# Performance work log

Hardware: AMD Instinct MI355X
Metric: run time of the kernel (lower is better)

## Reference

```python
import jax, jax.numpy as jnp
import numpy as np
from math import factorial

LMAX = 4
L2 = (LMAX + 1) ** 2                      # 25 spherical components
RES_B = 2 * (2 * LMAX + 1)                # 18 Gauss-Legendre beta nodes (exact for band 2*lmax products)
RES_A = 2 * (2 * LMAX + 1) + 1            # 19 uniform alpha nodes
EPS = 1e-5
# degree index of each (l,m) slot: [0,1,1,1,2,...]
L_IDX = np.repeat(np.arange(LMAX + 1), 2 * np.arange(LMAX + 1) + 1)


def _assoc_legendre(lmax, x):
    # Associated Legendre P_l^m(x) with Condon-Shortley phase; returns [l, m, B]
    B = x.shape[0]
    P = np.zeros((lmax + 1, lmax + 1, B))
    P[0, 0] = 1.0
    sx = np.sqrt(np.maximum(0.0, 1.0 - x * x))
    for m in range(1, lmax + 1):
        P[m, m] = -(2 * m - 1) * sx * P[m - 1, m - 1]
    for m in range(lmax):
        P[m + 1, m] = (2 * m + 1) * x * P[m, m]
    for m in range(lmax + 1):
        for l in range(m + 2, lmax + 1):
            P[l, m] = ((2 * l - 1) * x * P[l - 1, m] - (l + m - 1) * P[l - 2, m]) / (l - m)
    return P


def _build_sh(lmax, res_b, res_a):
    # Real orthonormal spherical harmonics sampled on a Gauss-Legendre x uniform-phi grid.
    ct, wb = np.polynomial.legendre.leggauss(res_b)       # cos(theta) nodes / weights
    phi = np.arange(res_a) * (2.0 * np.pi / res_a)
    P = _assoc_legendre(lmax, ct)
    l2 = (lmax + 1) ** 2
    Y = np.zeros((res_b, res_a, l2))
    for l in range(lmax + 1):
        for m in range(l + 1):
            Nlm = np.sqrt((2 * l + 1) / (4.0 * np.pi) * factorial(l - m) / factorial(l + m))
            if m == 0:
                Y[:, :, l * l + l] = (Nlm * P[l, 0])[:, None]
            else:
                base = np.sqrt(2.0) * Nlm * P[l, m]
                Y[:, :, l * l + l + m] = base[:, None] * np.cos(m * phi)[None, :]
                Y[:, :, l * l + l - m] = base[:, None] * np.sin(m * phi)[None, :]
    w = (wb[:, None] * np.full((1, res_a), 2.0 * np.pi / res_a)).reshape(-1)
    Yf = Y.reshape(-1, l2)
    return Yf, w

_Y_np, _w_np = _build_sh(LMAX, RES_B, RES_A)
TO_GRID = jnp.asarray(_Y_np, dtype=jnp.float32)                     # [G, L2]
FROM_GRID = jnp.asarray((_w_np[:, None] * _Y_np).T, dtype=jnp.float32)  # [L2, G], exact SH projection


def setup_inputs() -> dict:
    key = jax.random.key(0)
    ks = jax.random.split(key, 8)
    N, C = 6000, 128
    x = jax.random.normal(ks[0], (N, L2, C), dtype=jnp.float32)
    batch = jax.random.randint(ks[1], (N,), 0, 77)
    s = 1.0 / np.sqrt(C)
    return {
        "x": x,
        "batch": batch,
        "norm_w": jnp.ones((LMAX + 1, C), dtype=jnp.float32),
        "norm_b": jnp.zeros((C,), dtype=jnp.float32),
        "w1": jax.random.normal(ks[2], (LMAX + 1, C, C), dtype=jnp.float32) * s,
        "b1": jax.random.normal(ks[3], (C,), dtype=jnp.float32) * 0.02,
        "w_tp": jax.random.normal(ks[4], (LMAX + 1, C), dtype=jnp.float32),
        "w2": jax.random.normal(ks[5], (LMAX + 1, C, C), dtype=jnp.float32) * s,
        "b2": jax.random.normal(ks[6], (C,), dtype=jnp.float32) * 0.02,
    }


def _merge_layer_norm(x, w, b):
    # x: [N, L2, C]; center l=0 over channels, RMS over all components+channels, per-(l,C) affine.
    mean0 = jnp.mean(x[:, 0:1, :], axis=-1, keepdims=True)
    xc = jnp.concatenate([x[:, 0:1, :] - mean0, x[:, 1:, :]], axis=1)
    var = jnp.mean(xc * xc, axis=(1, 2), keepdims=True)
    xn = xc * jax.lax.rsqrt(var + EPS)
    out = xn * w[L_IDX][None]                      # [N, L2, C]
    return jnp.concatenate([out[:, 0:1, :] + b, out[:, 1:, :]], axis=1)


def _so3_linear(x, w, b):
    # per-degree linear: w [lmax+1, out, in]; bias on l=0 only
    W = w[L_IDX]                                    # [L2, out, in]
    y = jnp.einsum('nlc,lkc->nlk', x, W)
    return jnp.concatenate([y[:, 0:1, :] + b, y[:, 1:, :]], axis=1)


def _gaunt_self_tp(x, w_tp):
    # Gaunt self tensor-product (depthwise): pointwise square on the sphere,
    # exact projection back to SH (Gaunt-coefficient contraction), per-(l,C) weight.
    g = jnp.einsum('nlc,gl->ngc', x, TO_GRID)       # [N, G, C] to-grid
    y = jnp.einsum('ngc,lg->nlc', g * g, FROM_GRID)  # [N, L2, C] from-grid
    return y * w_tp[L_IDX][None]


def reference(x, batch, norm_w, norm_b, w1, b1, w_tp, w2, b2):
    x_res = x
    h = _merge_layer_norm(x, norm_w, norm_b)
    h = _so3_linear(h, w1, b1)
    h = _gaunt_self_tp(h, w_tp)
    h = _so3_linear(h, w2, b2)
    return h + x_res  # ffn_shortcut is Identity (num_in == num_out)
```

## Files before the change

### kernel.cpp

```cpp
#include <hip/hip_runtime.h>
#include <math.h>

#define L2C 25
#define CH  128
#define NB  8
#define GLB 7
#define GLA 13
#define NG  91
#define GPAD 96
#define KPAD 32
#define HROWS 242

typedef short bf16x8 __attribute__((ext_vector_type(8)));
typedef int   i32x4  __attribute__((ext_vector_type(4)));
typedef float f32x4  __attribute__((ext_vector_type(4)));
typedef unsigned uint2v __attribute__((ext_vector_type(2)));

union frag_u { i32x4 i; bf16x8 h; };

__device__ inline short f2bf(float f) {
  union { float f; unsigned u; } v; v.f = f;
  unsigned r = (v.u + 0x7FFFu + ((v.u >> 16) & 1u)) >> 16;
  return (short)r;
}
__device__ inline unsigned cvt_pk_bf16(float lo, float hi) {
  unsigned r; asm("v_cvt_pk_bf16_f32 %0, %1, %2" : "=v"(r) : "v"(lo), "v"(hi)); return r;
}

__global__ void build_tables_kernel(short* __restrict__ toT, short* __restrict__ frT) {
  const int g = threadIdx.x;
  if (g >= GPAD) return;
  const double PI = 3.14159265358979323846;
  double Y[L2C];
  double wg = 0.0;
  if (g < NG) {
    const int b = g / GLA;
    const int a = g % GLA;
    double xx = cos(PI * (b + 0.75) / (GLB + 0.5));
    double pp = 1.0;
    for (int it = 0; it < 64; ++it) {
      double p0 = 1.0, p1 = xx;
      for (int j = 2; j <= GLB; ++j) { double p2 = ((2.0*j-1.0)*xx*p1 - (j-1.0)*p0)/j; p0 = p1; p1 = p2; }
      pp = GLB * (xx*p1 - p0) / (xx*xx - 1.0);
      xx -= p1 / pp;
    }
    { double p0 = 1.0, p1 = xx;
      for (int j = 2; j <= GLB; ++j) { double p2 = ((2.0*j-1.0)*xx*p1 - (j-1.0)*p0)/j; p0 = p1; p1 = p2; }
      pp = GLB * (xx*p1 - p0) / (xx*xx - 1.0); }
    const double wb = 2.0 / ((1.0 - xx*xx) * pp * pp);
    const double ct = xx;
    const double sx = sqrt(fmax(0.0, 1.0 - ct*ct));
    double P[5][5];
    P[0][0] = 1.0;
    for (int m = 1; m <= 4; ++m) P[m][m] = -(2.0*m - 1.0) * sx * P[m-1][m-1];
    for (int m = 0; m <= 3; ++m) P[m+1][m] = (2.0*m + 1.0) * ct * P[m][m];
    for (int m = 0; m <= 4; ++m)
      for (int l = m + 2; l <= 4; ++l)
        P[l][m] = ((2.0*l-1.0)*ct*P[l-1][m] - (l+m-1.0)*P[l-2][m]) / (l - m);
    const double fact[9] = {1,1,2,6,24,120,720,5040,40320};
    const double phi = (2.0*PI/GLA) * a;
    for (int l = 0; l <= 4; ++l)
      for (int m = 0; m <= l; ++m) {
        double Nlm = sqrt((2.0*l+1.0)/(4.0*PI) * fact[l-m]/fact[l+m]);
        if (m == 0) Y[l*l + l] = Nlm * P[l][0];
        else {
          double base = sqrt(2.0) * Nlm * P[l][m];
          Y[l*l + l + m] = base * cos((double)m * phi);
          Y[l*l + l - m] = base * sin((double)m * phi);
        }
      }
    wg = wb * (2.0*PI/GLA);
  }
  for (int l = 0; l < KPAD; ++l) {
    float tv = (g < NG && l < L2C) ? (float)Y[l] : 0.f;
    toT[g*KPAD + l] = f2bf(tv);
  }
  {
    const int hi = g >> 4, r = g & 15;
    const int ksv = hi >> 1, pa = hi & 1;
    const int lqv = r >> 2,  pb = r & 3;
    const int kg = ksv*32 + lqv*8 + pa*4 + pb;
    for (int l = 0; l < KPAD; ++l)
      frT[l*GPAD + kg] = (g < NG && l < L2C) ? f2bf((float)(wg * Y[l])) : (short)0;
  }
}

__global__ void convert_w_kernel(const float* __restrict__ w1, const float* __restrict__ w2,
                                 short* __restrict__ wb1, short* __restrict__ wb2) {
  const int i = blockIdx.x * 256 + threadIdx.x;
  if (i < 5*CH*CH) { wb1[i] = f2bf(w1[i]); wb2[i] = f2bf(w2[i]); }
}

__global__ __launch_bounds__(512, 4) void eqv3_fused8u(
    const float* __restrict__ x,
    const float* __restrict__ norm_w, const float* __restrict__ norm_b,
    const short* __restrict__ wb1, const float* __restrict__ b1,
    const float* __restrict__ w_tp,
    const short* __restrict__ wb2, const float* __restrict__ b2,
    const short* __restrict__ toT, const short* __restrict__ frT,
    float* __restrict__ out)
{
  __shared__ __align__(16) short u[32768];
  short (*hsh)[HROWS][8] = (short (*)[HROWS][8])u;
  short (*hg)[4][CH][8]  = (short (*)[4][CH][8])u;

  const int tid  = threadIdx.x;
  const int w    = tid >> 6;
  const int lane = tid & 63;
  const int l16  = lane & 15;
  const int lq   = lane >> 4;
  const long n0  = (long)blockIdx.x * NB;
  const int k    = w*16 + l16;

  constexpr int LDEG[L2C] = {0,1,1,1,2,2,2,2,2,3,3,3,3,3,3,3,4,4,4,4,4,4,4,4,4};
  constexpr int BROW[5]   = {0,16,48,96,160};
  constexpr int NT[5]     = {1,2,3,4,5};

  {
    const float4* x4 = (const float4*)(x + (n0 + w)*(long)(L2C*CH));
    float4 xv[13];
    float s0 = 0.f, s0q = 0.f, sq = 0.f;
    #pragma unroll
    for (int it = 0; it < 13; ++it) {
      const int j = it*64 + lane;
      if (j < 800) {
        xv[it] = x4[j];
        const float t = xv[it].x*xv[it].x + xv[it].y*xv[it].y + xv[it].z*xv[it].z + xv[it].w*xv[it].w;
        if (j < 32) { s0 += xv[it].x + xv[it].y + xv[it].z + xv[it].w; s0q += t; }
        else        sq += t;
      }
    }
    #pragma unroll
    for (int o = 1; o < 64; o <<= 1) {
      s0  += __shfl_xor(s0,  o, 64);
      s0q += __shfl_xor(s0q, o, 64);
      sq  += __shfl_xor(sq,  o, 64);
    }
    const float mean0 = s0 * (1.f/CH);
    const float var   = (sq + s0q - CH*mean0*mean0) * (1.f/(L2C*CH));
    const float rstd  = rsqrtf(var + 1e-5f);
    #pragma unroll
    for (int it = 0; it < 13; ++it) {
      const int j = it*64 + lane;
      if (j < 800) {
        const int s = j >> 5;
        const int d = (int)sqrtf((float)s + 0.5f);
        const int row = 8*(s + d) + w;
        const int c32 = j & 31;
        const int c0  = c32 * 4;
        const float4 nw4 = ((const float4*)norm_w)[d*32 + c32];
        float a0 = xv[it].x, a1 = xv[it].y, a2 = xv[it].z, a3 = xv[it].w;
        if (s == 0) {
          const float4 nb4 = ((const float4*)norm_b)[c32];
          a0 = (a0 - mean0)*rstd*nw4.x + nb4.x;
          a1 = (a1 - mean0)*rstd*nw4.y + nb4.y;
          a2 = (a2 - mean0)*rstd*nw4.z + nb4.z;
          a3 = (a3 - mean0)*rstd*nw4.w + nb4.w;
        } else {
          a0 *= rstd*nw4.x; a1 *= rstd*nw4.y; a2 *= rstd*nw4.z; a3 *= rstd*nw4.w;
        }
        uint2v pk; pk[0] = cvt_pk_bf16(a0, a1); pk[1] = cvt_pk_bf16(a2, a3);
        *(uint2v*)&hsh[c0 >> 3][row][c0 & 7] = pk;
      }
    }
  }
  __syncthreads();

  unsigned pk1[15][2];
  {
    const float b1k = b1[k];
    int t = 0;
    #pragma unroll
    for (int d = 0; d < 5; ++d) {
      frag_u B[4];
      #pragma unroll
      for (int ks = 0; ks < 4; ++ks)
        B[ks].i = *(const i32x4*)(wb1 + ((d*CH + k)*CH + ks*32 + lq*8));
      #pragma unroll
      for (int mt = 0; mt < NT[d]; ++mt, ++t) {
        f32x4 acc = {0.f, 0.f, 0.f, 0.f};
        #pragma unroll
        for (int ks = 0; ks < 4; ++ks) {
          const bf16x8 a = *(const bf16x8*)&hsh[ks*4 + lq][BROW[d] + mt*16 + l16][0];
          acc = __builtin_amdgcn_mfma_f32_16x16x32_bf16(a, B[ks].h, acc, 0, 0, 0);
        }
        const int sl = 2*mt + (lq >> 1);
        const float bb = ((d == 0) & (sl == 0)) ? b1k : 0.f;
        pk1[t][0] = cvt_pk_bf16(acc[0] + bb, acc[1] + bb);
        pk1[t][1] = cvt_pk_bf16(acc[2] + bb, acc[3] + bb);
      }
    }
  }
  __syncthreads();

  {
    const i32x4 z = {0,0,0,0};
    #pragma unroll
    for (int n = 0; n < NB; ++n) *(i32x4*)&hg[n][3][k][0] = z;
    int t = 0;
    #pragma unroll
    for (int d = 0; d < 5; ++d)
      #pragma unroll
      for (int mt = 0; mt < NT[d]; ++mt, ++t) {
        const int sl = 2*mt + (lq >> 1);
        if (sl <= 2*d) {
          const int s  = d*d + sl;
          const int nb = (lq & 1)*4;
          hg[nb+0][s >> 3][k][s & 7] = (short)(pk1[t][0] & 0xFFFFu);
          hg[nb+1][s >> 3][k][s & 7] = (short)(pk1[t][0] >> 16);
          hg[nb+2][s >> 3][k][s & 7] = (short)(pk1[t][1] & 0xFFFFu);
          hg[nb+3][s >> 3][k][s & 7] = (short)(pk1[t][1] >> 16);
        }
      }
  }

  frag_u Bh[NB];
  #pragma unroll
  for (int n = 0; n < NB; ++n)
    Bh[n].i = *(const i32x4*)&hg[n][lq][k][0];
  __syncthreads();

  {
    frag_u Ato[6];
    #pragma unroll
    for (int gt = 0; gt < 6; ++gt)
      Ato[gt].i = *(const i32x4*)(toT + (gt*16 + l16)*KPAD + lq*8);
    frag_u Afr[2][3];
    #pragma unroll
    for (int mt = 0; mt < 2; ++mt)
      #pragma unroll
      for (int ks = 0; ks < 3; ++ks)
        Afr[mt][ks].i = *(const i32x4*)(frT + (mt*16 + l16)*GPAD + ks*32 + lq*8);

    float wtp[2][4]; int hrowb[2][4];
    #pragma unroll
    for (int mt = 0; mt < 2; ++mt)
      #pragma unroll
      for (int i = 0; i < 4; ++i) {
        const int l = mt*16 + lq*4 + i;
        if (l < L2C) {
          const int d = LDEG[l];
          wtp[mt][i]   = w_tp[d*CH + k];
          hrowb[mt][i] = BROW[d] + (l - d*d)*NB;
        } else { wtp[mt][i] = 0.f; hrowb[mt][i] = -1; }
      }

    #pragma unroll
    for (int np = 0; np < 4; ++np) {
      const int nA = np, nB2 = np + 4;
      unsigned pA[6][2], pB[6][2];
      #pragma unroll
      for (int gt = 0; gt < 6; ++gt) {
        f32x4 aA = {0.f,0.f,0.f,0.f}, aB = {0.f,0.f,0.f,0.f};
        aA = __builtin_amdgcn_mfma_f32_16x16x32_bf16(Ato[gt].h, Bh[nA].h,  aA, 0, 0, 0);
        aB = __builtin_amdgcn_mfma_f32_16x16x32_bf16(Ato[gt].h, Bh[nB2].h, aB, 0, 0, 0);
        pA[gt][0] = cvt_pk_bf16(aA[0]*aA[0], aA[1]*aA[1]);
        pA[gt][1] = cvt_pk_bf16(aA[2]*aA[2], aA[3]*aA[3]);
        pB[gt][0] = cvt_pk_bf16(aB[0]*aB[0], aB[1]*aB[1]);
        pB[gt][1] = cvt_pk_bf16(aB[2]*aB[2], aB[3]*aB[3]);
      }
      f32x4 acc2A[2] = {{0.f,0.f,0.f,0.f},{0.f,0.f,0.f,0.f}};
      f32x4 acc2B[2] = {{0.f,0.f,0.f,0.f},{0.f,0.f,0.f,0.f}};
      #pragma unroll
      for (int ks = 0; ks < 3; ++ks) {
        frag_u BgA, BgB;
        BgA.i[0] = (int)pA[2*ks][0];   BgA.i[1] = (int)pA[2*ks][1];
        BgA.i[2] = (int)pA[2*ks+1][0]; BgA.i[3] = (int)pA[2*ks+1][1];
        BgB.i[0] = (int)pB[2*ks][0];   BgB.i[1] = (int)pB[2*ks][1];
        BgB.i[2] = (int)pB[2*ks+1][0]; BgB.i[3] = (int)pB[2*ks+1][1];
        acc2A[0] = __builtin_amdgcn_mfma_f32_16x16x32_bf16(Afr[0][ks].h, BgA.h, acc2A[0], 0, 0, 0);
        acc2A[1] = __builtin_amdgcn_mfma_f32_16x16x32_bf16(Afr[1][ks].h, BgA.h, acc2A[1], 0, 0, 0);
        acc2B[0] = __builtin_amdgcn_mfma_f32_16x16x32_bf16(Afr[0][ks].h, BgB.h, acc2B[0], 0, 0, 0);
        acc2B[1] = __builtin_amdgcn_mfma_f32_16x16x32_bf16(Afr[1][ks].h, BgB.h, acc2B[1], 0, 0, 0);
      }
      #pragma unroll
      for (int mt = 0; mt < 2; ++mt)
        #pragma unroll
        for (int i = 0; i < 4; ++i)
          if (hrowb[mt][i] >= 0) {
            hsh[k >> 3][hrowb[mt][i] + nA][k & 7]  = f2bf(acc2A[mt][i] * wtp[mt][i]);
            hsh[k >> 3][hrowb[mt][i] + nB2][k & 7] = f2bf(acc2B[mt][i] * wtp[mt][i]);
          }
    }
  }
  __syncthreads();

  {
    const float b2k = b2[k];
    #pragma unroll
    for (int d = 0; d < 5; ++d) {
      frag_u B[4];
      #pragma unroll
      for (int ks = 0; ks < 4; ++ks)
        B[ks].i = *(const i32x4*)(wb2 + ((d*CH + k)*CH + ks*32 + lq*8));
      #pragma unroll
      for (int mt = 0; mt < NT[d]; ++mt) {
        f32x4 acc = {0.f, 0.f, 0.f, 0.f};
        #pragma unroll
        for (int ks = 0; ks < 4; ++ks) {
          const bf16x8 a = *(const bf16x8*)&hsh[ks*4 + lq][BROW[d] + mt*16 + l16][0];
          acc = __builtin_amdgcn_mfma_f32_16x16x32_bf16(a, B[ks].h, acc, 0, 0, 0);
        }
        const int sl = 2*mt + (lq >> 1);
        if (sl <= 2*d) {
          const int s = d*d + sl;
          #pragma unroll
          for (int i = 0; i < 4; ++i) {
            const int node = (lq & 1)*4 + i;
            const long base = (n0 + node)*(long)(L2C*CH) + s*CH + k;
            out[base] = acc[i] + ((s == 0) ? b2k : 0.f) + x[base];
          }
        }
      }
    }
  }
}

extern "C" void kernel_launch(void* const* d_in, const int* in_sizes, int n_in,
                              void* d_out, int out_size, void* d_ws, size_t ws_size,
                              hipStream_t stream) {
  const float* x      = (const float*)d_in[0];
  const float* norm_w = (const float*)d_in[2];
  const float* norm_b = (const float*)d_in[3];
  const float* w1     = (const float*)d_in[4];
  const float* b1     = (const float*)d_in[5];
  const float* w_tp   = (const float*)d_in[6];
  const float* w2     = (const float*)d_in[7];
  const float* b2     = (const float*)d_in[8];
  float* out = (float*)d_out;

  const int N = in_sizes[0] / (L2C*CH);

  short* wsS = (short*)d_ws;
  short* toT = wsS;
  short* frT = toT + GPAD*KPAD;
  short* wb1 = frT + KPAD*GPAD;
  short* wb2 = wb1 + 5*CH*CH;

  build_tables_kernel<<<1, 128, 0, stream>>>(toT, frT);
  convert_w_kernel<<<(5*CH*CH + 255)/256, 256, 0, stream>>>(w1, w2, wb1, wb2);
  eqv3_fused8u<<<N/NB, 512, 0, stream>>>(x, norm_w, norm_b, wb1, b1, w_tp, wb2, b2, toT, frT, out);
}
```

Before: 114.1 us.

## Process 16 nodes per block with one SH component per MFMA row tile

Doubles the nodes per workgroup from 8 to 16 and lays out the LDS tile so that each 16-row MFMA tile holds one spherical component across all 16 nodes. This removes the padded, wasted rows that the degree-grouped 8-node layout carried. It also halves the number of times the bf16 weight fragments are reloaded per node. The cost is double the LDS per block and a lower occupancy hint (2 blocks instead of 4), and with N=6000 there are only 375 blocks, which may underfill the GPU.

Measured after the change: 107.3 us. 1.06x faster.

```diff
diff --git a/kernel.cpp b/kernel.cpp
--- a/kernel.cpp
+++ b/kernel.cpp
@@ -3,13 +3,13 @@
 
 #define L2C 25
 #define CH  128
-#define NB  8
+#define NB  16
 #define GLB 7
 #define GLA 13
 #define NG  91
 #define GPAD 96
 #define KPAD 32
-#define HROWS 242
+#define HROWS 401
 
 typedef short bf16x8 __attribute__((ext_vector_type(8)));
 typedef int   i32x4  __attribute__((ext_vector_type(4)));
@@ -91,7 +91,7 @@
   if (i < 5*CH*CH) { wb1[i] = f2bf(w1[i]); wb2[i] = f2bf(w2[i]); }
 }
 
-__global__ __launch_bounds__(512, 4) void eqv3_fused8u(
+__global__ __launch_bounds__(512, 2) void eqv3_fused16(
     const float* __restrict__ x,
     const float* __restrict__ norm_w, const float* __restrict__ norm_b,
     const short* __restrict__ wb1, const float* __restrict__ b1,
@@ -100,7 +100,7 @@
     const short* __restrict__ toT, const short* __restrict__ frT,
     float* __restrict__ out)
 {
-  __shared__ __align__(16) short u[32768];
+  __shared__ __align__(16) short u[65536];
   short (*hsh)[HROWS][8] = (short (*)[HROWS][8])u;
   short (*hg)[4][CH][8]  = (short (*)[4][CH][8])u;
 
@@ -113,11 +113,12 @@
   const int k    = w*16 + l16;
 
   constexpr int LDEG[L2C] = {0,1,1,1,2,2,2,2,2,3,3,3,3,3,3,3,4,4,4,4,4,4,4,4,4};
-  constexpr int BROW[5]   = {0,16,48,96,160};
-  constexpr int NT[5]     = {1,2,3,4,5};
-
-  {
-    const float4* x4 = (const float4*)(x + (n0 + w)*(long)(L2C*CH));
+  constexpr int NT[5]     = {1,3,5,7,9};
+
+  #pragma unroll
+  for (int rep = 0; rep < 2; ++rep) {
+    const int node = w + rep*8;
+    const float4* x4 = (const float4*)(x + (n0 + node)*(long)(L2C*CH));
     float4 xv[13];
     float s0 = 0.f, s0q = 0.f, sq = 0.f;
     #pragma unroll
@@ -145,7 +146,7 @@
       if (j < 800) {
         const int s = j >> 5;
         const int d = (int)sqrtf((float)s + 0.5f);
-        const int row = 8*(s + d) + w;
+        const int row = 16*s + node;
         const int c32 = j & 31;
         const int c0  = c32 * 4;
         const float4 nw4 = ((const float4*)norm_w)[d*32 + c32];
@@ -166,10 +167,10 @@
   }
   __syncthreads();
 
-  unsigned pk1[15][2];
+  unsigned pk1[L2C][2];
   {
     const float b1k = b1[k];
-    int t = 0;
+    int s = 0;
     #pragma unroll
     for (int d = 0; d < 5; ++d) {
       frag_u B[4];
@@ -177,17 +178,16 @@
       for (int ks = 0; ks < 4; ++ks)
         B[ks].i = *(const i32x4*)(wb1 + ((d*CH + k)*CH + ks*32 + lq*8));
       #pragma unroll
-      for (int mt = 0; mt < NT[d]; ++mt, ++t) {
+      for (int mt = 0; mt < NT[d]; ++mt, ++s) {
         f32x4 acc = {0.f, 0.f, 0.f, 0.f};
         #pragma unroll
         for (int ks = 0; ks < 4; ++ks) {
-          const bf16x8 a = *(const bf16x8*)&hsh[ks*4 + lq][BROW[d] + mt*16 + l16][0];
+          const bf16x8 a = *(const bf16x8*)&hsh[ks*4 + lq][16*s + l16][0];
           acc = __builtin_amdgcn_mfma_f32_16x16x32_bf16(a, B[ks].h, acc, 0, 0, 0);
         }
-        const int sl = 2*mt + (lq >> 1);
-        const float bb = ((d == 0) & (sl == 0)) ? b1k : 0.f;
-        pk1[t][0] = cvt_pk_bf16(acc[0] + bb, acc[1] + bb);
-        pk1[t][1] = cvt_pk_bf16(acc[2] + bb, acc[3] + bb);
+        const float bb = (s == 0) ? b1k : 0.f;
+        pk1[s][0] = cvt_pk_bf16(acc[0] + bb, acc[1] + bb);
+        pk1[s][1] = cvt_pk_bf16(acc[2] + bb, acc[3] + bb);
       }
     }
   }
@@ -196,22 +196,16 @@
   {
     const i32x4 z = {0,0,0,0};
     #pragma unroll
-    for (int n = 0; n < NB; ++n) *(i32x4*)&hg[n][3][k][0] = z;
-    int t = 0;
-    #pragma unroll
-    for (int d = 0; d < 5; ++d)
-      #pragma unroll
-      for (int mt = 0; mt < NT[d]; ++mt, ++t) {
-        const int sl = 2*mt + (lq >> 1);
-        if (sl <= 2*d) {
-          const int s  = d*d + sl;
-          const int nb = (lq & 1)*4;
-          hg[nb+0][s >> 3][k][s & 7] = (short)(pk1[t][0] & 0xFFFFu);
-          hg[nb+1][s >> 3][k][s & 7] = (short)(pk1[t][0] >> 16);
-          hg[nb+2][s >> 3][k][s & 7] = (short)(pk1[t][1] & 0xFFFFu);
-          hg[nb+3][s >> 3][k][s & 7] = (short)(pk1[t][1] >> 16);
-        }
-      }
+    for (int j = 0; j < 4; ++j)
+      *(i32x4*)&hg[lq*4 + j][3][k][0] = z;
+    #pragma unroll
+    for (int s = 0; s < L2C; ++s) {
+      const int nb = lq*4;
+      hg[nb+0][s >> 3][k][s & 7] = (short)(pk1[s][0] & 0xFFFFu);
+      hg[nb+1][s >> 3][k][s & 7] = (short)(pk1[s][0] >> 16);
+      hg[nb+2][s >> 3][k][s & 7] = (short)(pk1[s][1] & 0xFFFFu);
+      hg[nb+3][s >> 3][k][s & 7] = (short)(pk1[s][1] >> 16);
+    }
   }
 
   frag_u Bh[NB];
@@ -239,15 +233,14 @@
       for (int i = 0; i < 4; ++i) {
         const int l = mt*16 + lq*4 + i;
         if (l < L2C) {
-          const int d = LDEG[l];
-          wtp[mt][i]   = w_tp[d*CH + k];
-          hrowb[mt][i] = BROW[d] + (l - d*d)*NB;
+          wtp[mt][i]   = w_tp[LDEG[l]*CH + k];
+          hrowb[mt][i] = 16*l;
         } else { wtp[mt][i] = 0.f; hrowb[mt][i] = -1; }
       }
 
     #pragma unroll
-    for (int np = 0; np < 4; ++np) {
-      const int nA = np, nB2 = np + 4;
+    for (int np = 0; np < 8; ++np) {
+      const int nA = np, nB2 = np + 8;
       unsigned pA[6][2], pB[6][2];
       #pragma unroll
       for (int gt = 0; gt < 6; ++gt) {
@@ -287,6 +280,7 @@
 
   {
     const float b2k = b2[k];
+    int s = 0;
     #pragma unroll
     for (int d = 0; d < 5; ++d) {
       frag_u B[4];
@@ -294,22 +288,19 @@
       for (int ks = 0; ks < 4; ++ks)
         B[ks].i = *(const i32x4*)(wb2 + ((d*CH + k)*CH + ks*32 + lq*8));
       #pragma unroll
-      for (int mt = 0; mt < NT[d]; ++mt) {
+      for (int mt = 0; mt < NT[d]; ++mt, ++s) {
         f32x4 acc = {0.f, 0.f, 0.f, 0.f};
         #pragma unroll
         for (int ks = 0; ks < 4; ++ks) {
-          const bf16x8 a = *(const bf16x8*)&hsh[ks*4 + lq][BROW[d] + mt*16 + l16][0];
+          const bf16x8 a = *(const bf16x8*)&hsh[ks*4 + lq][16*s + l16][0];
           acc = __builtin_amdgcn_mfma_f32_16x16x32_bf16(a, B[ks].h, acc, 0, 0, 0);
         }
-        const int sl = 2*mt + (lq >> 1);
-        if (sl <= 2*d) {
-          const int s = d*d + sl;
-          #pragma unroll
-          for (int i = 0; i < 4; ++i) {
-            const int node = (lq & 1)*4 + i;
-            const long base = (n0 + node)*(long)(L2C*CH) + s*CH + k;
-            out[base] = acc[i] + ((s == 0) ? b2k : 0.f) + x[base];
-          }
+        const float bb = (s == 0) ? b2k : 0.f;
+        #pragma unroll
+        for (int i = 0; i < 4; ++i) {
+          const int node = lq*4 + i;
+          const long base = (n0 + node)*(long)(L2C*CH) + s*CH + k;
+          out[base] = acc[i] + bb + x[base];
         }
       }
     }
@@ -339,5 +330,5 @@
 
   build_tables_kernel<<<1, 128, 0, stream>>>(toT, frT);
   convert_w_kernel<<<(5*CH*CH + 255)/256, 256, 0, stream>>>(w1, w2, wb1, wb2);
-  eqv3_fused8u<<<N/NB, 512, 0, stream>>>(x, norm_w, norm_b, wb1, b1, w_tp, wb2, b2, toT, frT, out);
-}
+  eqv3_fused16<<<N/NB, 512, 0, stream>>>(x, norm_w, norm_b, wb1, b1, w_tp, wb2, b2, toT, frT, out);
+}
```
